# Performance work log

Measured on AMD Instinct MI355X. Metric: run time of the kernel, lower is better.

## Reference

```python
import jax, jax.numpy as jnp
import numpy as np

B, S, D_IN, HEAD_DIM = 4, 4096, 1024, 128

def setup_inputs() -> dict:
    key = jax.random.key(0)
    k1, k2, k3, k4 = jax.random.split(key, 4)
    x = jax.random.normal(k1, (B, S, D_IN), dtype=jnp.float32)
    # nn.Parameter(torch.rand(...)) -> uniform [0,1)
    W_query = jax.random.uniform(k2, (D_IN, HEAD_DIM), dtype=jnp.float32)
    W_key = jax.random.uniform(k3, (D_IN, HEAD_DIM), dtype=jnp.float32)
    W_value = jax.random.uniform(k4, (D_IN, HEAD_DIM), dtype=jnp.float32)
    return {"x": x, "W_query": W_query, "W_key": W_key, "W_value": W_value}

def reference(x, W_query, W_key, W_value):
    # x: [B,S,d_in]; W_*: [d_in,head_dim]
    queries = jnp.einsum('bsd,dh->bsh', x, W_query)
    keys = jnp.einsum('bsd,dh->bsh', x, W_key)
    values = jnp.einsum('bsd,dh->bsh', x, W_value)
    scale = 1.0 / jnp.sqrt(jnp.asarray(HEAD_DIM, dtype=x.dtype))
    attn_scores = jnp.einsum('bqh,bkh->bqk', queries, keys)  # [B,S,S]
    attn_weights = jax.nn.softmax(attn_scores * scale, axis=-1)
    context_vec = jnp.einsum('bqk,bkh->bqh', attn_weights, values)
    return context_vec
```

## Files before the change

kernel.cpp:

```cpp
#include <hip/hip_runtime.h>
#include <cstdint>

#define B_  4
#define S_  4096
#define DIN 1024
#define DH  128
#define QSCALE (0.08838834764831845f * 1.4426950408889634f)

typedef short bf16x8 __attribute__((ext_vector_type(8)));
typedef float f32x4 __attribute__((ext_vector_type(4)));
typedef unsigned short u16;
typedef unsigned int   u32;

#define MFMA16(a, b, c) __builtin_amdgcn_mfma_f32_16x16x32_bf16(a, b, c, 0, 0, 0)

#define GLOAD_LDS16(g, l) __builtin_amdgcn_global_load_lds( \
    (const __attribute__((address_space(1))) void*)(g),     \
    (__attribute__((address_space(3))) void*)(l), 16, 0, 0)

#if __has_builtin(__builtin_amdgcn_exp2f)
#define EXP2(x) __builtin_amdgcn_exp2f(x)
#else
#define EXP2(x) exp2f(x)
#endif

__device__ inline u16 bf16_rn(float f) {
    union { float f; u32 u; } v; v.f = f;
    u32 r = v.u + 0x7FFFu + ((v.u >> 16) & 1u);
    return (u16)(r >> 16);
}
__device__ inline float bf16_f(u16 h) {
    union { u32 u; float f; } v; v.u = ((u32)h) << 16; return v.f;
}
__device__ inline u32 pk2(float a, float b) {
    u32 r;
    asm("v_cvt_pk_bf16_f32 %0, %1, %2" : "=v"(r) : "v"(a), "v"(b));
    return r;
}
__device__ inline void split2(float a, float b, u32& hi, u32& lo) {
    u32 ua = __builtin_bit_cast(u32, a), ub = __builtin_bit_cast(u32, b);
    u32 ha = ua & 0xFFFF0000u, hb = ub & 0xFFFF0000u;
    hi = (ua >> 16) | hb;
    float la = a - __builtin_bit_cast(float, ha);
    float lb = b - __builtin_bit_cast(float, hb);
    lo = (u32)bf16_rn(la) | ((u32)bf16_rn(lb) << 16);
}

__global__ __launch_bounds__(256) void wconv2(
    const float* __restrict__ Wq, const float* __restrict__ Wk, const float* __restrict__ Wv,
    u16* __restrict__ wpack)
{
    int id  = blockIdx.x * 256 + threadIdx.x;
    int s   = id / 2560;
    int rem = id % 2560;
    int p   = rem >> 9;
    int gi  = rem & 511;
    int n   = gi & 127, kq2 = gi >> 7;
    const float* W = (p < 2) ? Wq : (p < 4) ? Wk : Wv;
    int k0 = 32 * s + 8 * kq2;
    u16 o[8];
    #pragma unroll
    for (int j = 0; j < 8; ++j) {
        float v = W[(size_t)(k0 + j) * DH + n];
        if (p < 2) v *= QSCALE;
        if (p == 4) {
            o[j] = bf16_rn(v);
        } else {
            u32 u = __builtin_bit_cast(u32, v);
            if ((p & 1) == 0) o[j] = (u16)(u >> 16);
            else o[j] = bf16_rn(v - __builtin_bit_cast(float, u & 0xFFFF0000u));
        }
    }
    u16* dst = wpack + (size_t)id * 8;
    *(uint4*)dst = *(uint4*)o;
}

__global__ __launch_bounds__(512) void qkv_v8(
    const float* __restrict__ x, const u16* __restrict__ wpack,
    u16* __restrict__ qhi, u16* __restrict__ qlo,
    u16* __restrict__ khi, u16* __restrict__ klo, u16* __restrict__ vt)
{
    __shared__ __align__(16) char lds[81920];

    const int t    = threadIdx.x;
    const int row0 = blockIdx.x * 64;
    const int lane = t & 63, wave = t >> 6;
    const int l15  = lane & 15, g = lane >> 4;
    const int wr   = wave >> 1;
    const int wc   = wave & 1;

    f32x4 accq[4], acck[4], accv[4];
    #pragma unroll
    for (int nt = 0; nt < 4; ++nt)
        #pragma unroll
        for (int r = 0; r < 4; ++r) {
            accq[nt][r] = 0.f; acck[nt][r] = 0.f; accv[nt][r] = 0.f;
        }

    const char* WP = (const char*)wpack;
    auto stage = [&](int bufi, int s) {
        char* d = lds + bufi * 40960;
        const char* src = WP + (size_t)s * 40960;
        #pragma unroll
        for (int c = 0; c < 5; ++c) {
            int o = t * 16 + c * 8192;
            GLOAD_LDS16(src + o, d + o);
        }
    };

    const float* xp = x + (size_t)(row0 + 16 * wr + l15) * DIN + 8 * g;

    float4 ca = *(const float4*)(xp);
    float4 cb = *(const float4*)(xp + 4);

    stage(0, 0);
    __syncthreads();

    int buf = 0;
    for (int s = 0; s < 32; ++s) {
        if (s < 31) stage(buf ^ 1, s + 1);

        float4 na, nb;
        if (s < 31) {
            na = *(const float4*)(xp + 32 * (s + 1));
            nb = *(const float4*)(xp + 32 * (s + 1) + 4);
        }

        bf16x8 xh, xl;
        {
            uint4 H, L;
            split2(ca.x, ca.y, H.x, L.x); split2(ca.z, ca.w, H.y, L.y);
            split2(cb.x, cb.y, H.z, L.z); split2(cb.z, cb.w, H.w, L.w);
            xh = __builtin_bit_cast(bf16x8, H);
            xl = __builtin_bit_cast(bf16x8, L);
        }

        const char* wb = lds + buf * 40960;
        #pragma unroll
        for (int nt = 0; nt < 4; ++nt) {
            const int n  = 64 * wc + 16 * nt + l15;
            const int wo = (g << 11) + (n << 4);
            bf16x8 qwh = *(const bf16x8*)(wb + wo);
            bf16x8 qwl = *(const bf16x8*)(wb +  8192 + wo);
            bf16x8 kwh = *(const bf16x8*)(wb + 16384 + wo);
            bf16x8 kwl = *(const bf16x8*)(wb + 24576 + wo);
            bf16x8 vwh = *(const bf16x8*)(wb + 32768 + wo);
            accq[nt] = MFMA16(xh, qwh, accq[nt]);
            accq[nt] = MFMA16(xl, qwh, accq[nt]);
            accq[nt] = MFMA16(xh, qwl, accq[nt]);
            acck[nt] = MFMA16(xh, kwh, acck[nt]);
            acck[nt] = MFMA16(xl, kwh, acck[nt]);
            acck[nt] = MFMA16(xh, kwl, acck[nt]);
            accv[nt] = MFMA16(xh, vwh, accv[nt]);
        }
        __syncthreads();
        if (s < 31) { ca = na; cb = nb; }
        buf ^= 1;
    }

    const int bb = row0 >> 12, kt = (row0 & 4095) >> 6;

    #pragma unroll
    for (int reg = 0; reg < 4; ++reg) {
        int r = row0 + 16 * wr + 4 * g + reg;
        #pragma unroll
        for (int nt = 0; nt < 4; ++nt) {
            int c = 64 * wc + 16 * nt + l15;
            float v = accq[nt][reg];
            u32 u = __builtin_bit_cast(u32, v);
            float lo = v - __builtin_bit_cast(float, u & 0xFFFF0000u);
            size_t o = (size_t)r * DH + c;
            qhi[o] = (u16)(u >> 16);
            qlo[o] = bf16_rn(lo);
        }
    }

    u16* lk = (u16*)lds;
    #pragma unroll
    for (int reg = 0; reg < 4; ++reg) {
        int kr = 16 * wr + 4 * g + reg;
        #pragma unroll
        for (int nt = 0; nt < 4; ++nt) {
            int c = 64 * wc + 16 * nt + l15;
            int o = kr * 128 + (((c >> 3) ^ (kr & 15)) << 3) + (c & 7);
            float v = acck[nt][reg];
            u32 u = __builtin_bit_cast(u32, v);
            lk[o]        = (u16)(u >> 16);
            lk[8192 + o] = bf16_rn(v - __builtin_bit_cast(float, u & 0xFFFF0000u));
        }
    }
    __syncthreads();
    {
        char* gk = (char*)(khi + (size_t)(bb * 64 + kt) * 8192);
        char* gl = (char*)(klo + (size_t)(bb * 64 + kt) * 8192);
        #pragma unroll
        for (int c2 = 0; c2 < 2; ++c2) {
            int o = t * 16 + c2 * 8192;
            *(uint4*)(gk + o) = *(const uint4*)(lds + o);
            *(uint4*)(gl + o) = *(const uint4*)(lds + 16384 + o);
        }
    }
    __syncthreads();

    #pragma unroll
    for (int reg = 0; reg < 4; ++reg) {
        int kr = 16 * wr + 4 * g + reg;
        #pragma unroll
        for (int nt = 0; nt < 4; ++nt) {
            int c = 64 * wc + 16 * nt + l15;
            int o = c * 64 + (((kr >> 3) ^ (c & 7)) << 3) + (kr & 7);
            lk[o] = bf16_rn(accv[nt][reg]);
        }
    }
    __syncthreads();
    {
        char* gv = (char*)(vt + (size_t)(bb * 64 + kt) * 8192);
        #pragma unroll
        for (int c2 = 0; c2 < 2; ++c2) {
            int o = t * 16 + c2 * 8192;
            *(uint4*)(gv + o) = *(const uint4*)(lds + o);
        }
    }
}

__global__ __launch_bounds__(512, 2) void flash_db(
    const u16* __restrict__ qhi, const u16* __restrict__ qlo,
    const u16* __restrict__ khi, const u16* __restrict__ klo,
    const u16* __restrict__ vt,
    u16* __restrict__ opart, float2* __restrict__ ml)
{
    __shared__ __align__(16) char smem[2 * 49152];

    const int tid  = threadIdx.x;
    const int wave = tid >> 6, lane = tid & 63;
    const int l15  = lane & 15, g = lane >> 4;
    const int bid  = blockIdx.x;
    const int pair = bid & 15, qt = bid >> 4;
    const int b = pair >> 2, z = pair & 3;

    const int q0row = b * S_ + qt * 256 + wave * 32;

    bf16x8 qh[2][4], ql[2][4];
    #pragma unroll
    for (int h = 0; h < 2; ++h)
        #pragma unroll
        for (int ks = 0; ks < 4; ++ks) {
            size_t qa = (size_t)(q0row + 16 * h + l15) * DH + 32 * ks + 8 * g;
            qh[h][ks] = *(const bf16x8*)(qhi + qa);
            ql[h][ks] = *(const bf16x8*)(qlo + qa);
        }

    f32x4 O0[8], O1[8];
    #pragma unroll
    for (int dt = 0; dt < 8; ++dt)
        #pragma unroll
        for (int r = 0; r < 4; ++r) { O0[dt][r] = 0.f; O1[dt][r] = 0.f; }

    float m0 = -3.0e38f, l0 = 0.f, m1 = -3.0e38f, l1 = 0.f;

    int koff[4];
    #pragma unroll
    for (int ks = 0; ks < 4; ++ks)
        koff[ks] = (((4 * ks + g) ^ l15) << 4) + (l15 << 8);
    int voff[2];
    #pragma unroll
    for (int kw = 0; kw < 2; ++kw)
        voff[kw] = (((4 * kw + g) ^ (l15 & 7)) << 4);

    const char* kbase = (const char*)(khi + (size_t)b * 64 * 8192);
    const char* lbase = (const char*)(klo + (size_t)b * 64 * 8192);
    const char* vbase = (const char*)(vt  + (size_t)b * 64 * 8192);
    const int kt0 = z * 16;

    auto stage = [&](int bufi, int ktl) {
        const char* sk = kbase + (size_t)(kt0 + ktl) * 16384;
        const char* sl = lbase + (size_t)(kt0 + ktl) * 16384;
        const char* sv = vbase + (size_t)(kt0 + ktl) * 16384;
        char* dk = smem + bufi * 49152;
        #pragma unroll
        for (int c = 0; c < 2; ++c) {
            int o = tid * 16 + c * 8192;
            GLOAD_LDS16(sk + o, dk + o);
            GLOAD_LDS16(sl + o, dk + 16384 + o);
            GLOAD_LDS16(sv + o, dk + 32768 + o);
        }
    };

    stage(0, 0);
    __syncthreads();

    int buf = 0;
    for (int ktl = 0; ktl < 16; ++ktl) {
        if (ktl < 15) stage(buf ^ 1, ktl + 1);

        const char* bk = smem + buf * 49152;
        const char* bl = bk + 16384;
        const char* bv = bk + 32768;

        f32x4 s0[4], s1[4];
        #pragma unroll
        for (int nt = 0; nt < 4; ++nt)
            #pragma unroll
            for (int r = 0; r < 4; ++r) { s0[nt][r] = 0.f; s1[nt][r] = 0.f; }

        __builtin_amdgcn_s_setprio(1);
        #pragma unroll
        for (int ks = 0; ks < 4; ++ks) {
            #pragma unroll
            for (int nt = 0; nt < 4; ++nt) {
                bf16x8 kh = *(const bf16x8*)(bk + nt * 4096 + koff[ks]);
                bf16x8 kl = *(const bf16x8*)(bl + nt * 4096 + koff[ks]);
                s0[nt] = MFMA16(kh, qh[0][ks], s0[nt]);
                s0[nt] = MFMA16(kh, ql[0][ks], s0[nt]);
                s0[nt] = MFMA16(kl, qh[0][ks], s0[nt]);
                s1[nt] = MFMA16(kh, qh[1][ks], s1[nt]);
                s1[nt] = MFMA16(kh, ql[1][ks], s1[nt]);
                s1[nt] = MFMA16(kl, qh[1][ks], s1[nt]);
            }
        }
        __builtin_amdgcn_s_setprio(0);

        float ml0 = -3.0e38f, ml1 = -3.0e38f;
        #pragma unroll
        for (int nt = 0; nt < 4; ++nt)
            #pragma unroll
            for (int r = 0; r < 4; ++r) {
                ml0 = fmaxf(ml0, s0[nt][r]);
                ml1 = fmaxf(ml1, s1[nt][r]);
            }
        ml0 = fmaxf(ml0, __shfl_xor(ml0, 16));
        ml0 = fmaxf(ml0, __shfl_xor(ml0, 32));
        ml1 = fmaxf(ml1, __shfl_xor(ml1, 16));
        ml1 = fmaxf(ml1, __shfl_xor(ml1, 32));

        if (!__all((ml0 <= m0 + 8.0f) & (ml1 <= m1 + 8.0f))) {
            float mn0 = fmaxf(m0, ml0), mn1 = fmaxf(m1, ml1);
            float fsc0 = EXP2(m0 - mn0), fsc1 = EXP2(m1 - mn1);
            m0 = mn0; m1 = mn1;
            l0 *= fsc0; l1 *= fsc1;
            float fr0[4], fr1[4];
            #pragma unroll
            for (int r = 0; r < 4; ++r) {
                fr0[r] = __shfl(fsc0, 4 * g + r);
                fr1[r] = __shfl(fsc1, 4 * g + r);
            }
            #pragma unroll
            for (int dt = 0; dt < 8; ++dt)
                #pragma unroll
                for (int r = 0; r < 4; ++r) {
                    O0[dt][r] *= fr0[r];
                    O1[dt][r] *= fr1[r];
                }
        }

        u32 pk0[4][2], pk1[4][2];
        float ps0 = 0.f, ps1 = 0.f;
        #pragma unroll
        for (int nt = 0; nt < 4; ++nt) {
            float a0 = EXP2(s0[nt][0] - m0), a1 = EXP2(s0[nt][1] - m0);
            float a2 = EXP2(s0[nt][2] - m0), a3 = EXP2(s0[nt][3] - m0);
            ps0 += (a0 + a1) + (a2 + a3);
            pk0[nt][0] = pk2(a0, a1);
            pk0[nt][1] = pk2(a2, a3);
            float c0 = EXP2(s1[nt][0] - m1), c1 = EXP2(s1[nt][1] - m1);
            float c2 = EXP2(s1[nt][2] - m1), c3 = EXP2(s1[nt][3] - m1);
            ps1 += (c0 + c1) + (c2 + c3);
            pk1[nt][0] = pk2(c0, c1);
            pk1[nt][1] = pk2(c2, c3);
        }
        ps0 += __shfl_xor(ps0, 16);
        ps0 += __shfl_xor(ps0, 32);
        ps1 += __shfl_xor(ps1, 16);
        ps1 += __shfl_xor(ps1, 32);
        l0 += ps0; l1 += ps1;

        const int s0l = l15 | ((2 * (g & 1)) << 4);
        const int s1l = s0l + 16;
        const int hiH = g >> 1;
        #pragma unroll
        for (int kw = 0; kw < 2; ++kw) {
            u32 a0, a1, a2, a3, c0, c1, c2, c3;
            {
                u32 x0 = __shfl(pk0[2 * kw][0], s0l), y0 = __shfl(pk0[2 * kw + 1][0], s0l);
                u32 x1 = __shfl(pk0[2 * kw][1], s0l), y1 = __shfl(pk0[2 * kw + 1][1], s0l);
                u32 x2 = __shfl(pk0[2 * kw][0], s1l), y2 = __shfl(pk0[2 * kw + 1][0], s1l);
                u32 x3 = __shfl(pk0[2 * kw][1], s1l), y3 = __shfl(pk0[2 * kw + 1][1], s1l);
                a0 = hiH ? y0 : x0; a1 = hiH ? y1 : x1;
                a2 = hiH ? y2 : x2; a3 = hiH ? y3 : x3;
            }
            {
                u32 x0 = __shfl(pk1[2 * kw][0], s0l), y0 = __shfl(pk1[2 * kw + 1][0], s0l);
                u32 x1 = __shfl(pk1[2 * kw][1], s0l), y1 = __shfl(pk1[2 * kw + 1][1], s0l);
                u32 x2 = __shfl(pk1[2 * kw][0], s1l), y2 = __shfl(pk1[2 * kw + 1][0], s1l);
                u32 x3 = __shfl(pk1[2 * kw][1], s1l), y3 = __shfl(pk1[2 * kw + 1][1], s1l);
                c0 = hiH ? y0 : x0; c1 = hiH ? y1 : x1;
                c2 = hiH ? y2 : x2; c3 = hiH ? y3 : x3;
            }
            union { u32 w[4]; bf16x8 v; } pa, pb;
            pa.w[0] = a0; pa.w[1] = a1; pa.w[2] = a2; pa.w[3] = a3;
            pb.w[0] = c0; pb.w[1] = c1; pb.w[2] = c2; pb.w[3] = c3;
            __builtin_amdgcn_s_setprio(1);
            #pragma unroll
            for (int dt = 0; dt < 8; ++dt) {
                bf16x8 vf = *(const bf16x8*)(bv + (16 * dt + l15) * 128 + voff[kw]);
                O0[dt] = MFMA16(pa.v, vf, O0[dt]);
                O1[dt] = MFMA16(pb.v, vf, O1[dt]);
            }
            __builtin_amdgcn_s_setprio(0);
        }

        __syncthreads();
        buf ^= 1;
    }

    u16* op = opart + ((size_t)z * 16384 + q0row) * DH;
    #pragma unroll
    for (int dt = 0; dt < 8; ++dt)
        #pragma unroll
        for (int r = 0; r < 4; ++r) {
            op[(size_t)(4 * g + r) * DH + 16 * dt + l15]      = bf16_rn(O0[dt][r]);
            op[(size_t)(16 + 4 * g + r) * DH + 16 * dt + l15] = bf16_rn(O1[dt][r]);
        }
    if (lane < 16) {
        ml[(size_t)z * 16384 + q0row + lane]      = make_float2(m0, l0);
        ml[(size_t)z * 16384 + q0row + 16 + lane] = make_float2(m1, l1);
    }
}

__global__ __launch_bounds__(256) void merge4(
    const u16* __restrict__ op, const float2* __restrict__ ml, float* __restrict__ O)
{
    int row = blockIdx.x * 16 + (threadIdx.x >> 4);
    int dq  = (threadIdx.x & 15) * 8;
    float2 a[4];
    #pragma unroll
    for (int zz = 0; zz < 4; ++zz) a[zz] = ml[(size_t)zz * 16384 + row];
    float M = fmaxf(fmaxf(a[0].x, a[1].x), fmaxf(a[2].x, a[3].x));
    float w[4], den = 0.f;
    #pragma unroll
    for (int zz = 0; zz < 4; ++zz) {
        w[zz] = EXP2(a[zz].x - M);
        den += a[zz].y * w[zz];
    }
    float inv = 1.0f / den;
    float acc[8];
    #pragma unroll
    for (int j = 0; j < 8; ++j) acc[j] = 0.f;
    #pragma unroll
    for (int zz = 0; zz < 4; ++zz) {
        const u16* p = op + ((size_t)zz * 16384 + row) * DH + dq;
        bf16x8 vv = *(const bf16x8*)p;
        #pragma unroll
        for (int j = 0; j < 8; ++j) acc[j] += w[zz] * bf16_f((u16)vv[j]);
    }
    float4 oa, ob;
    oa.x = acc[0] * inv; oa.y = acc[1] * inv; oa.z = acc[2] * inv; oa.w = acc[3] * inv;
    ob.x = acc[4] * inv; ob.y = acc[5] * inv; ob.z = acc[6] * inv; ob.w = acc[7] * inv;
    *(float4*)(O + (size_t)row * DH + dq)     = oa;
    *(float4*)(O + (size_t)row * DH + dq + 4) = ob;
}

extern "C" void kernel_launch(void* const* d_in, const int* in_sizes, int n_in,
                              void* d_out, int out_size, void* d_ws, size_t ws_size,
                              hipStream_t stream) {
    const float* x  = (const float*)d_in[0];
    const float* Wq = (const float*)d_in[1];
    const float* Wk = (const float*)d_in[2];
    const float* Wv = (const float*)d_in[3];
    float* out = (float*)d_out;

    const size_t SZ = (size_t)B_ * S_ * DH;
    u16* qhi = (u16*)d_ws;
    u16* qlo = qhi + SZ;
    u16* khi = qlo + SZ;
    u16* klo = khi + SZ;
    u16* vtp = klo + SZ;
    u16* wpk = vtp + SZ;
    u16* opart = wpk + 655360;
    float2* mlp = (float2*)((char*)opart + (size_t)4 * 16384 * DH * 2);

    wconv2<<<320, 256, 0, stream>>>(Wq, Wk, Wv, wpk);
    qkv_v8<<<256, 512, 0, stream>>>(x, wpk, qhi, qlo, khi, klo, vtp);
    flash_db<<<256, 512, 0, stream>>>(qhi, qlo, khi, klo, vtp, opart, mlp);
    merge4<<<1024, 256, 0, stream>>>(opart, mlp, out);
}
```

Baseline: 126.9 us.

## Software-pipeline flash attention: overlap next tile's QK with current softmax-PV

Restructures the flash kernel into a triple-buffered LDS pipeline, computing QK^T scores for tile k+1 before running softmax and PV for tile k. Loads are issued two tiles ahead. The aim is to let the independent QK MFMAs overlap the softmax/shuffle latency and the PV phase. In exchange, LDS grows from 96KB to 144KB per block, and keeping two sets of score accumulators raises register pressure. Under launch_bounds(512,2) that may cut occupancy to one block per CU or cause spills.

```diff
diff --git a/kernel.cpp b/kernel.cpp
--- a/kernel.cpp
+++ b/kernel.cpp
@@ -223,13 +223,13 @@
     }
 }
 
-__global__ __launch_bounds__(512, 2) void flash_db(
+__global__ __launch_bounds__(512, 2) void flash_p(
     const u16* __restrict__ qhi, const u16* __restrict__ qlo,
     const u16* __restrict__ khi, const u16* __restrict__ klo,
     const u16* __restrict__ vt,
     u16* __restrict__ opart, float2* __restrict__ ml)
 {
-    __shared__ __align__(16) char smem[2 * 49152];
+    __shared__ __align__(16) char smem[3 * 49152];
 
     const int tid  = threadIdx.x;
     const int wave = tid >> 6, lane = tid & 63;
@@ -272,11 +272,10 @@
     const char* vbase = (const char*)(vt  + (size_t)b * 64 * 8192);
     const int kt0 = z * 16;
 
-    auto stage = [&](int bufi, int ktl) {
+    auto stage = [&](char* dk, int ktl) {
         const char* sk = kbase + (size_t)(kt0 + ktl) * 16384;
         const char* sl = lbase + (size_t)(kt0 + ktl) * 16384;
         const char* sv = vbase + (size_t)(kt0 + ktl) * 16384;
-        char* dk = smem + bufi * 49152;
         #pragma unroll
         for (int c = 0; c < 2; ++c) {
             int o = tid * 16 + c * 8192;
@@ -286,23 +285,12 @@
         }
     };
 
-    stage(0, 0);
-    __syncthreads();
-
-    int buf = 0;
-    for (int ktl = 0; ktl < 16; ++ktl) {
-        if (ktl < 15) stage(buf ^ 1, ktl + 1);
-
-        const char* bk = smem + buf * 49152;
+    auto qk = [&](f32x4* s0, f32x4* s1, const char* bk) {
         const char* bl = bk + 16384;
-        const char* bv = bk + 32768;
-
-        f32x4 s0[4], s1[4];
         #pragma unroll
         for (int nt = 0; nt < 4; ++nt)
             #pragma unroll
             for (int r = 0; r < 4; ++r) { s0[nt][r] = 0.f; s1[nt][r] = 0.f; }
-
         __builtin_amdgcn_s_setprio(1);
         #pragma unroll
         for (int ks = 0; ks < 4; ++ks) {
@@ -319,7 +307,9 @@
             }
         }
         __builtin_amdgcn_s_setprio(0);
-
+    };
+
+    auto smpv = [&](f32x4* s0, f32x4* s1, const char* bv) {
         float ml0 = -3.0e38f, ml1 = -3.0e38f;
         #pragma unroll
         for (int nt = 0; nt < 4; ++nt)
@@ -408,9 +398,32 @@
             }
             __builtin_amdgcn_s_setprio(0);
         }
-
+    };
+
+    char* pc = smem;
+    char* pn = smem + 49152;
+    char* pf = smem + 2 * 49152;
+    stage(pc, 0);
+    stage(pn, 1);
+    __syncthreads();
+
+    f32x4 sE0[4], sE1[4], sO0[4], sO1[4];
+    qk(sE0, sE1, pc);
+
+    for (int tt = 0; tt < 8; ++tt) {
+        if (tt < 7) stage(pf, 2 * tt + 2);
+        qk(sO0, sO1, pn);
+        smpv(sE0, sE1, pc + 32768);
         __syncthreads();
-        buf ^= 1;
+        { char* tmp = pc; pc = pn; pn = pf; pf = tmp; }
+
+        if (tt < 7) {
+            stage(pf, 2 * tt + 3);
+            qk(sE0, sE1, pn);
+        }
+        smpv(sO0, sO1, pc + 32768);
+        __syncthreads();
+        { char* tmp = pc; pc = pn; pn = pf; pf = tmp; }
     }
 
     u16* op = opart + ((size_t)z * 16384 + q0row) * DH;
@@ -481,6 +494,6 @@
 
     wconv2<<<320, 256, 0, stream>>>(Wq, Wk, Wv, wpk);
     qkv_v8<<<256, 512, 0, stream>>>(x, wpk, qhi, qlo, khi, klo, vtp);
-    flash_db<<<256, 512, 0, stream>>>(qhi, qlo, khi, klo, vtp, opart, mlp);
+    flash_p<<<256, 512, 0, stream>>>(qhi, qlo, khi, klo, vtp, opart, mlp);
     merge4<<<1024, 256, 0, stream>>>(opart, mlp, out);
 }
```

Measured after the change: 141.2 us. 11.3% more time.
